# Performance work log

Hardware: AMD Instinct MI355X
Metric: run time of the kernel (lower is better)

Reference implementation:

```python
import jax, jax.numpy as jnp
import numpy as np
import math


def sinusoidal_embedding(n_pos, d_model, dtype=jnp.float32):
    # matches SpaceEmbedding: se[:,0::2]=sin(pos*div), se[:,1::2]=cos(pos*div)
    pos = jnp.arange(n_pos, dtype=dtype)[:, None]                      # [T,1]
    div = jnp.exp(jnp.arange(0, d_model, 2, dtype=dtype) * (-math.log(10000.0) / d_model))  # [d/2]
    ang = pos * div                                                    # [T,d/2]
    se = jnp.stack([jnp.sin(ang), jnp.cos(ang)], axis=-1).reshape(n_pos, d_model)
    return se


def setup_inputs() -> dict:
    key = jax.random.key(0)
    ks = jax.random.split(key, 6)
    B, D_in, T, d = 32, 512, 1024, 1024
    s_in = 1.0 / np.sqrt(D_in)
    s_d = 1.0 / np.sqrt(d)
    return {
        "xs": jax.random.normal(ks[0], (B, D_in, T), dtype=jnp.float32),
        "W_embed": jax.random.uniform(ks[1], (d, D_in), minval=-s_in, maxval=s_in, dtype=jnp.float32),
        "W_KQ": jax.random.uniform(ks[2], (d, d), minval=-s_d, maxval=s_d, dtype=jnp.float32),
        "W_PV": jax.random.uniform(ks[3], (d, d), minval=-s_d, maxval=s_d, dtype=jnp.float32),
        "W_un": jax.random.uniform(ks[4], (D_in, d), minval=-s_d, maxval=s_d, dtype=jnp.float32),
        "b_un": jnp.zeros((D_in,), dtype=jnp.float32),
    }


def reference(xs, W_embed, W_KQ, W_PV, W_un, b_un):
    B, D_in, T = xs.shape
    d = W_embed.shape[0]
    rho = 1.0
    # patch embedding: Linear(dim_input, d_model, bias=False) on [B,T,D_in]
    patch = jnp.einsum('bnt,dn->btd', xs, W_embed)                     # [B,T,d]
    emb = patch + sinusoidal_embedding(T, d, patch.dtype)[None]        # [B,T,d]
    E = jnp.transpose(emb, (0, 2, 1))                                  # [B,d,T]
    X = E[:, :, :-1]                                                   # [B,d,T-1] (skip last token)
    # attn_arg = X^T @ W_KQ @ E / rho  -> [B,T-1,T]
    attn_arg = jnp.einsum('bdm,de,bet->bmt', X, W_KQ, E) / rho
    soft = jax.nn.softmax(attn_arg, axis=1)                            # softmax over T-1 (keys) dim
    # f_attn = W_PV @ X @ soft -> [B,d,T]
    f_attn = jnp.einsum('de,bem,bmt->bdt', W_PV, X, soft)
    # unembed: Linear(d_model, dim_input) applied to [B,T,d], then transpose back
    out_full = jnp.einsum('bdt,od->bot', f_attn, W_un) + b_un[None, :, None]  # [B,D_in,T]
    return out_full, attn_arg
```

## Files before the change

kernel.cpp:

```cpp
#include <hip/hip_runtime.h>
#include <hip/hip_bf16.h>
#include <cstdio>

typedef __bf16 bf16;
typedef __bf16 bf16x4 __attribute__((ext_vector_type(4)));
typedef __bf16 bf16x8 __attribute__((ext_vector_type(8)));
typedef float  f32x4  __attribute__((ext_vector_type(4)));

#define AS1 __attribute__((address_space(1)))
#define AS3 __attribute__((address_space(3)))

__device__ __forceinline__ void async16(void* lds, const void* g) {
    __builtin_amdgcn_global_load_lds((AS1 unsigned int*)g, (AS3 unsigned int*)lds, 16, 0, 0);
}

enum { EPI_NONE = 0, EPI_SINUS = 1, EPI_BIAS = 2, EPI_ATTN = 3 };

#define FENCE asm volatile("" ::: "memory")
#define BAR   do { FENCE; __builtin_amdgcn_s_barrier(); FENCE; } while (0)
#define LGKM0 do { asm volatile("s_waitcnt lgkmcnt(0)" ::: "memory"); \
                   __builtin_amdgcn_sched_barrier(0); } while (0)
#define RD8(p) (*(const bf16x8*)(const void*)(p))

#define MFMA_Q(AF, MB, BF, NB)                                                 \
    _Pragma("unroll") for (int mf = 0; mf < 4; ++mf)                           \
    _Pragma("unroll") for (int nf = 0; nf < 2; ++nf)                           \
    _Pragma("unroll") for (int s = 0; s < 2; ++s)                              \
        acc[(MB) + mf][(NB) + nf] = __builtin_amdgcn_mfma_f32_16x16x32_bf16(   \
            AF[mf][s], BF[nf][s], acc[(MB) + mf][(NB) + nf], 0, 0, 0);

__device__ __forceinline__ void onl_merge(float& mx, float& sm, float omx, float osm) {
    float nm = fmaxf(mx, omx);
    sm = sm * __expf(mx - nm) + osm * __expf(omx - nm);
    mx = nm;
}

template <int EPI, typename CT>
__launch_bounds__(512, 2)
__global__ void gemm8(const bf16* __restrict__ A, long sA, int lda,
                      const bf16* __restrict__ B, long sB, int ldb,
                      CT* __restrict__ C, long sC, int ldc,
                      int K, int mLimit, const float* __restrict__ bias,
                      float* __restrict__ pmx, float* __restrict__ psum,
                      int tilesM, int tilesN)
{
    __shared__ __align__(16) char smem[131072];
    char* ldsA = smem;
    char* ldsB = smem + 65536;

    const int tid  = threadIdx.x;
    const int wave = tid >> 6;
    const int lane = tid & 63;
    const int quad = lane >> 4;
    const int l16  = lane & 15;
    const int hw   = wave >> 2;
    const int wq   = wave & 3;
    const int hbB  = wq >> 1;
    const int rrB  = (wq & 1) * 64;

    const int nwg = gridDim.x;
    const int qq = nwg >> 3, rr = nwg & 7;
    const int xcd = blockIdx.x & 7, idx = blockIdx.x >> 3;
    const int wgid = (xcd < rr ? xcd * (qq + 1) : rr * (qq + 1) + (xcd - rr) * qq) + idx;

    const int tpb = tilesM * tilesN;
    const int b   = wgid / tpb;
    const int rem = wgid - b * tpb;
    const int m0  = (rem / tilesN) * 256;
    const int n0  = (rem % tilesN) * 256;

    A += (long)b * sA;
    B += (long)b * sB;

    const int odt  = wave * 1024 + lane * 16;
    const int ol   = odt ^ (((odt >> 7) & 7) << 4);
    const int srow = ol >> 7;
    const int scol = (ol & 127) >> 1;
    const bf16* pA = A + (long)(m0 + srow) * lda + scol;
    const bf16* pB = B + (long)(n0 + srow) * ldb + scol;

    const int xr = (l16 & 7) << 4;
    const int lane2_0 = ((l16 * 128) + (quad * 16)) ^ xr;
    const int lane2_1 = ((l16 * 128) + 64 + (quad * 16)) ^ xr;

    auto stgA = [&](int bb, int h, int kt) {
        char* l = ldsA + bb * 32768 + h * 16384 + wave * 1024;
        const bf16* g = pA + (long)(h * 128) * lda + kt * 64;
        async16(l, g);
        async16(l + 8192, g + (long)64 * lda);
    };
    auto stgB = [&](int bb, int h, int kt) {
        char* l = ldsB + bb * 32768 + h * 16384 + wave * 1024;
        const bf16* g = pB + (long)(h * 128) * ldb + kt * 64;
        async16(l, g);
        async16(l + 8192, g + (long)64 * ldb);
    };

    const int nk = K >> 6;

    stgA(0, 0, 0); stgA(0, 1, 0);
    stgB(0, 0, 0); stgB(0, 1, 0);
    stgA(1, 0, 1); stgA(1, 1, 1);
    asm volatile("s_waitcnt vmcnt(4)" ::: "memory");
    BAR;

    f32x4 acc[8][4] = {};

    for (int t = 0; t < nk; ++t) {
        const int cur = t & 1;
        const char* aH = ldsA + cur * 32768 + hw * 16384;
        const char* bH = ldsB + cur * 32768 + hbB * 16384 + rrB * 128;

        bf16x8 af03[4][2], af47[4][2], bf01[2][2], bf23[2][2];

        #pragma unroll
        for (int mf = 0; mf < 4; ++mf) {
            af03[mf][0] = RD8(aH + mf * 2048 + lane2_0);
            af03[mf][1] = RD8(aH + mf * 2048 + lane2_1);
        }
        #pragma unroll
        for (int nf = 0; nf < 2; ++nf) {
            bf01[nf][0] = RD8(bH + nf * 2048 + lane2_0);
            bf01[nf][1] = RD8(bH + nf * 2048 + lane2_1);
        }
        if (t + 1 < nk) stgB(cur ^ 1, 0, t + 1);
        BAR;
        LGKM0;
        __builtin_amdgcn_s_setprio(1);
        MFMA_Q(af03, 0, bf01, 0);
        __builtin_amdgcn_s_setprio(0);
        BAR;

        #pragma unroll
        for (int nf = 0; nf < 2; ++nf) {
            bf23[nf][0] = RD8(bH + (nf + 2) * 2048 + lane2_0);
            bf23[nf][1] = RD8(bH + (nf + 2) * 2048 + lane2_1);
        }
        if (t + 1 < nk) stgB(cur ^ 1, 1, t + 1);
        BAR;
        LGKM0;
        __builtin_amdgcn_s_setprio(1);
        MFMA_Q(af03, 0, bf23, 2);
        __builtin_amdgcn_s_setprio(0);
        BAR;

        #pragma unroll
        for (int mf = 0; mf < 4; ++mf) {
            af47[mf][0] = RD8(aH + (mf + 4) * 2048 + lane2_0);
            af47[mf][1] = RD8(aH + (mf + 4) * 2048 + lane2_1);
        }
        if (t + 2 < nk) stgA(cur, 0, t + 2);
        BAR;
        LGKM0;
        __builtin_amdgcn_s_setprio(1);
        MFMA_Q(af47, 4, bf01, 0);
        __builtin_amdgcn_s_setprio(0);
        BAR;

        if (t + 2 < nk) {
            stgA(cur, 1, t + 2);
            asm volatile("s_waitcnt vmcnt(4)" ::: "memory");
        } else {
            asm volatile("s_waitcnt vmcnt(0)" ::: "memory");
        }
        BAR;
        __builtin_amdgcn_s_setprio(1);
        MFMA_Q(af47, 4, bf23, 2);
        __builtin_amdgcn_s_setprio(0);
        BAR;
    }

    C += (long)b * sC;

    #pragma unroll
    for (int nf = 0; nf < 4; ++nf) {
        const int col = n0 + wq * 64 + nf * 16 + l16;
        float fr = 0.f;
        if (EPI == EPI_SINUS)
            fr = __expf((float)(-(col & ~1)) * (9.210340371976184f / 1024.f));
        #pragma unroll
        for (int mf = 0; mf < 8; ++mf) {
            #pragma unroll
            for (int r = 0; r < 4; ++r) {
                const int row = m0 + hw * 128 + mf * 16 + quad * 4 + r;
                float v = acc[mf][nf][r];
                if (EPI == EPI_SINUS) {
                    float ang = (float)row * fr;
                    v += (col & 1) ? __cosf(ang) : __sinf(ang);
                }
                if (EPI == EPI_BIAS) v += bias[row];
                if (row < mLimit)
                    C[(long)row * ldc + col] = (CT)v;
            }
        }
    }

    if (EPI == EPI_ATTN) {
        float nmx[4], nsm[4];
        #pragma unroll
        for (int nf = 0; nf < 4; ++nf) {
            float mx = -1e30f;
            #pragma unroll
            for (int mf = 0; mf < 8; ++mf)
                #pragma unroll
                for (int r = 0; r < 4; ++r) {
                    const int row = m0 + hw * 128 + mf * 16 + quad * 4 + r;
                    float v = (row < mLimit) ? acc[mf][nf][r] : -1e30f;
                    mx = fmaxf(mx, v);
                }
            float sm = 0.f;
            #pragma unroll
            for (int mf = 0; mf < 8; ++mf)
                #pragma unroll
                for (int r = 0; r < 4; ++r) {
                    const int row = m0 + hw * 128 + mf * 16 + quad * 4 + r;
                    float v = (row < mLimit) ? acc[mf][nf][r] : -1e30f;
                    sm += __expf(v - mx);
                }
            float omx = __shfl_xor(mx, 16), osm = __shfl_xor(sm, 16);
            onl_merge(mx, sm, omx, osm);
            omx = __shfl_xor(mx, 32); osm = __shfl_xor(sm, 32);
            onl_merge(mx, sm, omx, osm);
            nmx[nf] = mx; nsm[nf] = sm;
        }
        float smx = quad == 0 ? nmx[0] : quad == 1 ? nmx[1] : quad == 2 ? nmx[2] : nmx[3];
        float ssm = quad == 0 ? nsm[0] : quad == 1 ? nsm[1] : quad == 2 ? nsm[2] : nsm[3];
        float2* red = (float2*)smem;
        red[wave * 64 + lane] = make_float2(smx, ssm);
        __syncthreads();
        if (wave < 4) {
            float2 x = red[wave * 64 + lane];
            float2 y = red[(wave + 4) * 64 + lane];
            onl_merge(x.x, x.y, y.x, y.y);
            const int col = n0 + wq * 64 + lane;
            const int mt  = m0 >> 8;
            pmx [((long)b * 4 + mt) * 1024 + col] = x.x;
            psum[((long)b * 4 + mt) * 1024 + col] = x.y;
        }
    }
}

__launch_bounds__(256)
__global__ void cvt_f32_bf16(const float* __restrict__ in, bf16* __restrict__ out, int n)
{
    int i = (blockIdx.x * 256 + threadIdx.x) * 4;
    if (i < n) {
        float4 v = *(const float4*)(in + i);
        out[i]     = (bf16)v.x;
        out[i + 1] = (bf16)v.y;
        out[i + 2] = (bf16)v.z;
        out[i + 3] = (bf16)v.w;
    }
}

__launch_bounds__(256)
__global__ void transpose_f32_bf16(const float* __restrict__ in, bf16* __restrict__ out,
                                   int rows, int cols)
{
    __shared__ float tile[32][33];
    const long bs = (long)rows * cols;
    in  += (long)blockIdx.z * bs;
    out += (long)blockIdx.z * bs;
    const int c0 = blockIdx.x * 32, r0 = blockIdx.y * 32;
    const int tx = threadIdx.x, ty = threadIdx.y;
    #pragma unroll
    for (int i = ty; i < 32; i += 8)
        tile[i][tx] = in[(long)(r0 + i) * cols + c0 + tx];
    __syncthreads();
    #pragma unroll
    for (int i = ty; i < 32; i += 8)
        out[(long)(c0 + i) * rows + r0 + tx] = (bf16)tile[tx][i];
}

__launch_bounds__(256)
__global__ void transpose_bf16(const bf16* __restrict__ in, bf16* __restrict__ out,
                               int rows, int cols)
{
    __shared__ bf16 tile[32][33];
    const long bs = (long)rows * cols;
    in  += (long)blockIdx.z * bs;
    out += (long)blockIdx.z * bs;
    const int c0 = blockIdx.x * 32, r0 = blockIdx.y * 32;
    const int tx = threadIdx.x, ty = threadIdx.y;
    #pragma unroll
    for (int i = ty; i < 32; i += 8)
        tile[i][tx] = in[(long)(r0 + i) * cols + c0 + tx];
    __syncthreads();
    #pragma unroll
    for (int i = ty; i < 32; i += 8)
        out[(long)(c0 + i) * rows + r0 + tx] = tile[tx][i];
}

__launch_bounds__(256)
__global__ void softmax_norm_T(const float* __restrict__ attn,
                               const float* __restrict__ pmx,
                               const float* __restrict__ psum,
                               bf16* __restrict__ softT)
{
    __shared__ bf16 tile[64][66];
    const int b  = blockIdx.z;
    const int mt = blockIdx.x;
    const int ct = blockIdx.y;
    const int tx = threadIdx.x & 63;
    const int ty = threadIdx.x >> 6;
    const int col = ct * 64 + tx;

    float MX = -1e30f, SM = 0.f;
    #pragma unroll
    for (int p = 0; p < 4; ++p) {
        float omx = pmx [((long)b * 4 + p) * 1024 + col];
        float osm = psum[((long)b * 4 + p) * 1024 + col];
        onl_merge(MX, SM, omx, osm);
    }
    const float INV = 1.f / SM;

    const float* a = attn + (long)b * (1023l * 1024);
    const int m0 = mt * 64;
    #pragma unroll
    for (int i = ty; i < 64; i += 4) {
        const int m = m0 + i;
        float p = 0.f;
        if (m < 1023) p = __expf(a[(long)m * 1024 + col] - MX) * INV;
        tile[tx][i] = (bf16)p;
    }
    __syncthreads();
    bf16* o = softT + (long)b * (1024l * 1024) + (long)(ct * 64) * 1024 + m0;
    #pragma unroll
    for (int j = ty; j < 64; j += 4)
        o[(long)j * 1024 + tx] = tile[j][tx];
}

extern "C" void kernel_launch(void* const* d_in, const int* in_sizes, int n_in,
                              void* d_out, int out_size, void* d_ws, size_t ws_size,
                              hipStream_t stream)
{
    const float* xs    = (const float*)d_in[0];
    const float* W_emb = (const float*)d_in[1];
    const float* W_KQ  = (const float*)d_in[2];
    const float* W_PV  = (const float*)d_in[3];
    const float* W_un  = (const float*)d_in[4];
    const float* b_un  = (const float*)d_in[5];

    float* out  = (float*)d_out;
    float* attn = out + (size_t)32 * 512 * 1024;

    const long MB = 1024l * 1024;

    char* ws = (char*)d_ws;
    const size_t oXsT  = 0;
    const size_t oET   = oXsT + (size_t)33554432;
    const size_t oEn   = oET  + (size_t)67108864;
    const size_t oQT   = oEn  + (size_t)67108864;
    const size_t oR    = oQT  + (size_t)67108864;
    const size_t oWe   = oR   + (size_t)67108864;
    const size_t oWkq  = oWe  + (size_t)1048576;
    const size_t oWpv  = oWkq + (size_t)2097152;
    const size_t oWun  = oWpv + (size_t)2097152;
    const size_t need  = oWun + (size_t)1048576;
    if (ws_size < need) { fprintf(stderr, "ws too small: %zu < %zu\n", ws_size, need); return; }

    bf16* xsT   = (bf16*)(ws + oXsT);
    bf16* ET    = (bf16*)(ws + oET);
    bf16* En    = (bf16*)(ws + oEn);
    bf16* QT    = (bf16*)(ws + oQT);
    bf16* We    = (bf16*)(ws + oWe);
    bf16* Wkq   = (bf16*)(ws + oWkq);
    bf16* Wpv   = (bf16*)(ws + oWpv);
    bf16* Wun   = (bf16*)(ws + oWun);
    bf16* softT = QT;
    bf16* A1T   = (bf16*)(ws + oR);
    bf16* fT    = ET;

    float* pmx  = (float*)(ws + oR);
    float* psum = pmx + (size_t)32 * 4 * 1024;

    const dim3 tb(32, 8);
    const int BIG = 1 << 30;

    cvt_f32_bf16<<<512, 256, 0, stream>>>(W_emb, We, 524288);
    cvt_f32_bf16<<<1024, 256, 0, stream>>>(W_KQ, Wkq, 1048576);
    cvt_f32_bf16<<<1024, 256, 0, stream>>>(W_PV, Wpv, 1048576);
    cvt_f32_bf16<<<512, 256, 0, stream>>>(W_un, Wun, 524288);
    transpose_f32_bf16<<<dim3(32, 16, 32), tb, 0, stream>>>(xs, xsT, 512, 1024);
    gemm8<EPI_SINUS, bf16><<<dim3(512), 512, 0, stream>>>(
        xsT, 512l * 1024, 512, We, 0, 512, ET, MB, 1024, 512, BIG, nullptr, nullptr, nullptr, 4, 4);
    transpose_bf16<<<dim3(32, 32, 32), tb, 0, stream>>>(ET, En, 1024, 1024);
    gemm8<EPI_NONE, bf16><<<dim3(512), 512, 0, stream>>>(
        ET, MB, 1024, Wkq, 0, 1024, QT, MB, 1024, 1024, BIG, nullptr, nullptr, nullptr, 4, 4);
    gemm8<EPI_ATTN, float><<<dim3(512), 512, 0, stream>>>(
        ET, MB, 1024, QT, MB, 1024, attn, 1023l * 1024, 1024, 1024, 1023, nullptr, pmx, psum, 4, 4);
    softmax_norm_T<<<dim3(16, 16, 32), 256, 0, stream>>>(attn, pmx, psum, softT);
    gemm8<EPI_NONE, bf16><<<dim3(512), 512, 0, stream>>>(
        softT, MB, 1024, En, MB, 1024, A1T, MB, 1024, 1024, BIG, nullptr, nullptr, nullptr, 4, 4);
    gemm8<EPI_NONE, bf16><<<dim3(512), 512, 0, stream>>>(
        A1T, MB, 1024, Wpv, 0, 1024, fT, MB, 1024, 1024, BIG, nullptr, nullptr, nullptr, 4, 4);
    gemm8<EPI_BIAS, float><<<dim3(256), 512, 0, stream>>>(
        Wun, 0, 1024, fT, MB, 1024, out, 512l * 1024, 1024, 1024, BIG, b_un, nullptr, nullptr, 2, 4);
}
```

Before: 801.1 us.

## Fold W_PV into unembedding weight to drop a per-batch GEMM

Precomputes Wc = W_un · W_PV once with a new small NT GEMM kernel, then applies Wc directly to the attention output. This removes the batched 32×1024×1024×1024 GEMM with W_PV and its intermediate write. The cost is an extra transpose and a small weight GEMM, plus slightly different bf16 rounding because the combined weight is rounded once. The LGKM0 macro also loses its sched_barrier.

```diff
diff --git a/kernel.cpp b/kernel.cpp
--- a/kernel.cpp
+++ b/kernel.cpp
@@ -18,8 +18,7 @@
 
 #define FENCE asm volatile("" ::: "memory")
 #define BAR   do { FENCE; __builtin_amdgcn_s_barrier(); FENCE; } while (0)
-#define LGKM0 do { asm volatile("s_waitcnt lgkmcnt(0)" ::: "memory"); \
-                   __builtin_amdgcn_sched_barrier(0); } while (0)
+#define LGKM0 asm volatile("s_waitcnt lgkmcnt(0)" ::: "memory")
 #define RD8(p) (*(const bf16x8*)(const void*)(p))
 
 #define MFMA_Q(AF, MB, BF, NB)                                                 \
@@ -240,6 +239,84 @@
     }
 }
 
+constexpr int BM = 128, BN = 128, BK = 32;
+template <int EPI, typename CT>
+__launch_bounds__(256)
+__global__ void gemm_nt(const bf16* __restrict__ A, long sA, int lda,
+                        const bf16* __restrict__ B, long sB, int ldb,
+                        CT* __restrict__ C, long sC, int ldc,
+                        int K, int mLimit,
+                        const float* __restrict__ bias)
+{
+    __shared__ __align__(16) bf16 As[BM * BK];
+    __shared__ __align__(16) bf16 Bs[BN * BK];
+
+    const int tid  = threadIdx.x;
+    const int wave = tid >> 6;
+    const int lane = tid & 63;
+    const int quad = lane >> 4;
+    const int l16  = lane & 15;
+    const int b    = blockIdx.z;
+    const int m0   = blockIdx.y * BM;
+    const int n0   = blockIdx.x * BN;
+
+    A += (long)b * sA;
+    B += (long)b * sB;
+
+    const int srow = lane >> 2;
+    const int scol = (lane & 3) * 8;
+    const bf16* gA = A + (long)(m0 + wave * 32 + srow) * lda + scol;
+    const bf16* gB = B + (long)(n0 + wave * 32 + srow) * ldb + scol;
+    char* lA = (char*)As + wave * 2048;
+    char* lB = (char*)Bs + wave * 2048;
+
+    const int wm = (wave >> 1) * 64;
+    const int wn = (wave & 1) * 64;
+
+    f32x4 acc[4][4] = {};
+
+    for (int k0 = 0; k0 < K; k0 += BK) {
+        __syncthreads();
+        async16(lA,        gA);
+        async16(lA + 1024, gA + (long)16 * lda);
+        async16(lB,        gB);
+        async16(lB + 1024, gB + (long)16 * ldb);
+        gA += BK; gB += BK;
+        __syncthreads();
+
+        bf16x8 af[4], bfr[4];
+        #pragma unroll
+        for (int i = 0; i < 4; i++) {
+            af[i]  = *(const bf16x8*)(As + (wm + i * 16 + l16) * BK + quad * 8);
+            bfr[i] = *(const bf16x8*)(Bs + (wn + i * 16 + l16) * BK + quad * 8);
+        }
+        #pragma unroll
+        for (int mi = 0; mi < 4; mi++)
+            #pragma unroll
+            for (int ni = 0; ni < 4; ni++)
+                acc[mi][ni] = __builtin_amdgcn_mfma_f32_16x16x32_bf16(
+                    af[mi], bfr[ni], acc[mi][ni], 0, 0, 0);
+    }
+
+    C += (long)b * sC;
+
+    #pragma unroll
+    for (int ni = 0; ni < 4; ni++) {
+        const int col = n0 + wn + ni * 16 + l16;
+        #pragma unroll
+        for (int mi = 0; mi < 4; mi++) {
+            #pragma unroll
+            for (int r = 0; r < 4; r++) {
+                const int row = m0 + wm + mi * 16 + quad * 4 + r;
+                float v = acc[mi][ni][r];
+                if (EPI == EPI_BIAS) v += bias[row];
+                if (row < mLimit)
+                    C[(long)row * ldc + col] = (CT)v;
+            }
+        }
+    }
+}
+
 __launch_bounds__(256)
 __global__ void cvt_f32_bf16(const float* __restrict__ in, bf16* __restrict__ out, int n)
 {
@@ -354,9 +431,10 @@
     const size_t oR    = oQT  + (size_t)67108864;
     const size_t oWe   = oR   + (size_t)67108864;
     const size_t oWkq  = oWe  + (size_t)1048576;
-    const size_t oWpv  = oWkq + (size_t)2097152;
-    const size_t oWun  = oWpv + (size_t)2097152;
-    const size_t need  = oWun + (size_t)1048576;
+    const size_t oWpvT = oWkq + (size_t)2097152;
+    const size_t oWun  = oWpvT + (size_t)2097152;
+    const size_t oWc   = oWun + (size_t)1048576;
+    const size_t need  = oWc  + (size_t)1048576;
     if (ws_size < need) { fprintf(stderr, "ws too small: %zu < %zu\n", ws_size, need); return; }
 
     bf16* xsT   = (bf16*)(ws + oXsT);
@@ -365,11 +443,11 @@
     bf16* QT    = (bf16*)(ws + oQT);
     bf16* We    = (bf16*)(ws + oWe);
     bf16* Wkq   = (bf16*)(ws + oWkq);
-    bf16* Wpv   = (bf16*)(ws + oWpv);
+    bf16* WpvT  = (bf16*)(ws + oWpvT);
     bf16* Wun   = (bf16*)(ws + oWun);
+    bf16* Wc    = (bf16*)(ws + oWc);
     bf16* softT = QT;
     bf16* A1T   = (bf16*)(ws + oR);
-    bf16* fT    = ET;
 
     float* pmx  = (float*)(ws + oR);
     float* psum = pmx + (size_t)32 * 4 * 1024;
@@ -379,8 +457,10 @@
 
     cvt_f32_bf16<<<512, 256, 0, stream>>>(W_emb, We, 524288);
     cvt_f32_bf16<<<1024, 256, 0, stream>>>(W_KQ, Wkq, 1048576);
-    cvt_f32_bf16<<<1024, 256, 0, stream>>>(W_PV, Wpv, 1048576);
     cvt_f32_bf16<<<512, 256, 0, stream>>>(W_un, Wun, 524288);
+    transpose_f32_bf16<<<dim3(32, 32, 1), tb, 0, stream>>>(W_PV, WpvT, 1024, 1024);
+    gemm_nt<EPI_NONE, bf16><<<dim3(8, 4, 1), 256, 0, stream>>>(
+        Wun, 0, 1024, WpvT, 0, 1024, Wc, 0, 1024, 1024, BIG, nullptr);
     transpose_f32_bf16<<<dim3(32, 16, 32), tb, 0, stream>>>(xs, xsT, 512, 1024);
     gemm8<EPI_SINUS, bf16><<<dim3(512), 512, 0, stream>>>(
         xsT, 512l * 1024, 512, We, 0, 512, ET, MB, 1024, 512, BIG, nullptr, nullptr, nullptr, 4, 4);
@@ -392,8 +472,6 @@
     softmax_norm_T<<<dim3(16, 16, 32), 256, 0, stream>>>(attn, pmx, psum, softT);
     gemm8<EPI_NONE, bf16><<<dim3(512), 512, 0, stream>>>(
         softT, MB, 1024, En, MB, 1024, A1T, MB, 1024, 1024, BIG, nullptr, nullptr, nullptr, 4, 4);
-    gemm8<EPI_NONE, bf16><<<dim3(512), 512, 0, stream>>>(
-        A1T, MB, 1024, Wpv, 0, 1024, fT, MB, 1024, 1024, BIG, nullptr, nullptr, nullptr, 4, 4);
     gemm8<EPI_BIAS, float><<<dim3(256), 512, 0, stream>>>(
-        Wun, 0, 1024, fT, MB, 1024, out, 512l * 1024, 1024, 1024, BIG, b_un, nullptr, nullptr, 2, 4);
-}
+        Wc, 0, 1024, A1T, MB, 1024, out, 512l * 1024, 1024, 1024, BIG, b_un, nullptr, nullptr, 2, 4);
+}
```

New measurement: 744.5 us. -7.1%, faster.
